# Performance work log

Measured on AMD Instinct MI355X. Metric: run time of the kernel, lower is better.

## Reference

```python
import jax, jax.numpy as jnp
import numpy as np
from jax import lax

MAX_C = 16       # MAX_MERGE_NUMS
COND_THRES = 0.2
IOU_THRES = 0.3
CLASS_OFFSET = 1e4  # shift per-class so cross-class BEV IoU == 0 (emulates per-class loop)


def setup_inputs() -> dict:
    key = jax.random.key(0)
    k1, k2, k3, k4, k5 = jax.random.split(key, 5)
    B, N = 4, 4096
    # realistic 3D boxes: centers, positive sizes, heading
    centers = jax.random.normal(k1, (B, N, 3), jnp.float32) * 20.0
    sizes = jax.random.uniform(k2, (B, N, 3), jnp.float32, 0.5, 4.5)
    heading = jax.random.uniform(k3, (B, N, 1), jnp.float32, -np.pi, np.pi)
    boxes = jnp.concatenate([centers, sizes, heading], -1)  # [B,N,7]
    scores = jax.random.uniform(k4, (B, N), jnp.float32)
    labels = jax.random.randint(k5, (B, N), 0, 3, jnp.int32)
    kw = jax.random.split(jax.random.fold_in(key, 1), 2)
    W1 = jax.random.normal(kw[0], (7, 64), jnp.float32) * 0.3
    b1 = jnp.zeros((64,), jnp.float32)
    W2 = jax.random.normal(kw[1], (64, 1), jnp.float32) * 0.3
    b2 = jnp.zeros((1,), jnp.float32)
    return {"boxes": boxes, "scores": scores, "labels": labels,
            "W1": W1, "b1": b1, "W2": W2, "b2": b2}


def _nms_merge_frame(boxes, scores, labels, W1, b1, W2, b2):
    # boxes [N,7], scores [N], labels [N] int32
    N = boxes.shape[0]
    valid = scores > COND_THRES                       # cond_mask
    skey = jnp.where(valid, scores, -jnp.inf)
    order = jnp.argsort(-skey)                        # score descending
    boxes, scores = boxes[order], scores[order]
    labels, valid = labels[order], valid[order]

    # nearest-BEV (axis-aligned) IoU; class offset keeps classes disjoint
    off = labels.astype(boxes.dtype) * CLASS_OFFSET
    cx, cy = boxes[:, 0] + off, boxes[:, 1]
    hx, hy = boxes[:, 3] * 0.5, boxes[:, 4] * 0.5
    x1, x2, y1, y2 = cx - hx, cx + hx, cy - hy, cy + hy
    ix = jnp.clip(jnp.minimum(x2[:, None], x2[None]) - jnp.maximum(x1[:, None], x1[None]), 0.0)
    iy = jnp.clip(jnp.minimum(y2[:, None], y2[None]) - jnp.maximum(y1[:, None], y1[None]), 0.0)
    inter = ix * iy                                   # [N,N]
    area = (x2 - x1) * (y2 - y1)
    iou = inter / jnp.clip(area[:, None] + area[None] - inter, 1e-6)
    overlap = iou > IOU_THRES                         # includes self

    # greedy clustering: highest-score remaining box leads its cluster
    def body(i, st):
        alive, cid = st
        lead = alive[i]
        take = alive & overlap[i] & lead
        cid = jnp.where(take, i, cid)
        return alive & (~take), cid
    alive, cid = lax.fori_loop(0, N, body,
                               (valid, jnp.full((N,), -1, jnp.int32)))
    leader = cid == jnp.arange(N, dtype=jnp.int32)    # cluster representatives

    # rank of each box within its cluster (score order preserved)
    idx = jnp.arange(N)
    same = (cid[None, :] == cid[:, None]) & (cid[:, None] >= 0)
    rank = (same & (idx[None, :] < idx[:, None])).sum(-1)  # [N]

    # scatter up to MAX_C members per cluster (zero-padded buffers)
    dest = jnp.where((cid >= 0) & (rank < MAX_C), cid, N)  # N = dump row
    clusters = jnp.zeros((N + 1, MAX_C, 7), boxes.dtype)
    clusters = clusters.at[dest, jnp.minimum(rank, MAX_C - 1)].set(boxes)[:N]

    # merge network: per-box MLP -> softmax weights over cluster slots
    h = jax.nn.relu(clusters @ W1 + b1)               # [N,MAX_C,64]
    logits = (h @ W2 + b2)[..., 0]                    # [N,MAX_C]
    slot_ok = jnp.any(clusters != 0, -1)
    logits = jnp.where(slot_ok, logits, -1e9)
    w = jax.nn.softmax(logits, -1)
    merged = jnp.einsum('nc,ncd->nd', w, clusters)    # [N,7]

    # masked scatter: non-positive merged sizes fall back to leader sizes
    size = jnp.where(merged[:, 3:6] <= 0, boxes[:, 3:6], merged[:, 3:6])
    out_box = jnp.concatenate([merged[:, :3], size, merged[:, 6:7]], -1)
    info = jnp.concatenate([out_box, scores[:, None],
                            labels.astype(boxes.dtype)[:, None]], -1)  # [N,9]
    info = jnp.where(leader[:, None], info, 0.0)
    return info, leader


def reference(boxes, scores, labels, W1, b1, W2, b2):
    info, leader = jax.vmap(_nms_merge_frame,
                            in_axes=(0, 0, 0, None, None, None, None))(
        boxes, scores, labels, W1, b1, W2, b2)
    return info, leader
```

## Files before the change

### kernel.cpp

```cpp
#include <hip/hip_runtime.h>
#include <stdint.h>

#pragma clang fp contract(off)

#define BF 4
#define NN 4096
#define MAXC 16
#define PL 2048
#define WL 32
#define WF 24
#define TRI_CAP (64 * (WL * (WL + 1) / 2))

typedef unsigned long long u64;
typedef uint32_t u32;

#define WAVE_SYNC() asm volatile("s_waitcnt lgkmcnt(0)" ::: "memory")

__device__ __forceinline__ u64 shfl64(u64 v, int src) {
  return (u64)__shfl((long long)v, src, 64);
}
__device__ __forceinline__ u64 readlane64(u64 v, int l) {
  u32 lo = (u32)__builtin_amdgcn_readlane((int)(u32)v, l);
  u32 hi = (u32)__builtin_amdgcn_readlane((int)(u32)(v >> 32), l);
  return ((u64)hi << 32) | lo;
}
__device__ __forceinline__ u64 greedy64_iso(u64 D, u64 rem, u64 onlyme) {
  u64 lead = 0;
  while (rem) {
    u64 t = D & rem;
    u64 iso = __ballot(t == onlyme) & rem;
    lead |= iso;
    rem &= ~iso;
    if (!rem) break;
    int b = __builtin_ctzll(rem);
    lead |= 1ull << b;
    rem &= ~readlane64(D, b);
    if (!rem) break;
    b = __builtin_ctzll(rem);
    lead |= 1ull << b;
    rem &= ~readlane64(D, b);
  }
  return lead;
}

__global__ __launch_bounds__(256) void rg_kernel(
    const float* __restrict__ scores, const float* __restrict__ boxes,
    const int* __restrict__ labels,
    float* __restrict__ sboxes, float* __restrict__ sscore, float* __restrict__ slabel,
    int* __restrict__ lab_slot, int* __restrict__ loc_slot,
    int* __restrict__ pglob,
    float* __restrict__ px1, float* __restrict__ px2, float* __restrict__ py1,
    float* __restrict__ py2, float* __restrict__ parea,
    int* __restrict__ VbufL)
{
  __shared__ u64 keys[NN];
  __shared__ int cnt[4][64];
  __shared__ int lcnt[4][64];
  __shared__ int vc[4][3];
  const int f = blockIdx.x >> 6, rb = blockIdx.x & 63;
  const int tid = threadIdx.x, wave = tid >> 6, lane = tid & 63;
  for (int s = 0; s < 16; s++) {
    int idx = tid + 256 * s;
    float sc = scores[f * NN + idx];
    bool valid = sc > 0.2f;
    int lab = labels[f * NN + idx];
    u32 bits = __float_as_uint(sc);
    u32 m = bits ^ ((bits >> 31) ? 0xFFFFFFFFu : 0x80000000u);
    u32 hi = valid ? ~m : 0xFFFFFFFFu;
    u32 lo = ((u32)idx << 2) | (valid ? (u32)lab : 3u);
    keys[idx] = ((u64)hi << 32) | lo;
  }
  __syncthreads();
  if (rb == 0) {
    int c0 = 0, c1 = 0, c2 = 0;
    const int base = wave * 1024;
    for (int s = 0; s < 16; s++) {
      u32 lb = (u32)keys[base + s * 64 + lane] & 3u;
      c0 += (lb == 0); c1 += (lb == 1); c2 += (lb == 2);
    }
    for (int off = 32; off; off >>= 1) {
      c0 += __shfl_xor(c0, off, 64);
      c1 += __shfl_xor(c1, off, 64);
      c2 += __shfl_xor(c2, off, 64);
    }
    if (lane == 0) { vc[wave][0] = c0; vc[wave][1] = c1; vc[wave][2] = c2; }
  }
  const int row = rb * 64 + lane;
  const u64 mykey = keys[row];
  const u32 mylab = (u32)mykey & 3u;
  int c = 0, lc = 0;
  const int j0 = wave * 1024;
#pragma unroll 8
  for (int j = j0; j < j0 + 1024; j++) {
    u64 kj = keys[j];
    bool lt = kj < mykey;
    c += lt ? 1 : 0;
    lc += (lt && (((u32)kj & 3u) == mylab)) ? 1 : 0;
  }
  cnt[wave][lane] = c;
  lcnt[wave][lane] = lc;
  __syncthreads();
  if (rb == 0 && wave == 1 && lane < 3)
    VbufL[f * 3 + lane] = vc[0][lane] + vc[1][lane] + vc[2][lane] + vc[3][lane];
  if (wave == 0) {
    int rank = cnt[0][lane] + cnt[1][lane] + cnt[2][lane] + cnt[3][lane];
    int loc  = lcnt[0][lane] + lcnt[1][lane] + lcnt[2][lane] + lcnt[3][lane];
    const int i = row;
    const float* bp = boxes + (size_t)(f * NN + i) * 7;
    float b0 = bp[0], b1v = bp[1], b2v = bp[2], b3 = bp[3], b4 = bp[4], b5 = bp[5], b6 = bp[6];
    int lab = labels[f * NN + i];
    float sc = scores[f * NN + i];
    const int o = f * NN + rank;
    float* sb = sboxes + (size_t)o * 7;
    sb[0] = b0; sb[1] = b1v; sb[2] = b2v; sb[3] = b3; sb[4] = b4; sb[5] = b5; sb[6] = b6;
    sscore[o] = sc;
    slabel[o] = (float)lab;
    if (mylab < 3u) {
      int pi = (f * 3 + (int)mylab) * PL + loc;
      float off = (float)mylab * 10000.0f;
      float cx = b0 + off, cy = b1v;
      float hx = b3 * 0.5f, hy = b4 * 0.5f;
      float x1 = cx - hx, x2 = cx + hx, y1 = cy - hy, y2 = cy + hy;
      float area = (x2 - x1) * (y2 - y1);
      pglob[pi] = rank;
      px1[pi] = x1; px2[pi] = x2; py1[pi] = y1; py2[pi] = y2; parea[pi] = area;
      lab_slot[o] = (int)mylab; loc_slot[o] = loc;
    } else {
      lab_slot[o] = -1; loc_slot[o] = -1;
    }
  }
}

__global__ __launch_bounds__(256) void mask_kernel(
    const float* __restrict__ px1, const float* __restrict__ px2,
    const float* __restrict__ py1, const float* __restrict__ py2,
    const float* __restrict__ parea, const int* __restrict__ pglob,
    const int* __restrict__ VbufL,
    u64* __restrict__ maskP, u64* __restrict__ triT)
{
  __shared__ float4 cbox[1024];
  __shared__ float carea[1024];
  const int bx = blockIdx.x;
  const int fl = bx >> 8, rem = bx & 255;
  const int rt = rem >> 1, wt = rem & 1;
  const int r0 = rt * 16;
  const int Vl = VbufL[fl];
  if (r0 >= Vl) return;
  if (wt * 1024 >= Vl) return;
  const int tid = threadIdx.x;
  const int ncol = Vl - wt * 1024;
  const int nload = (ncol < 1024) ? ncol : 1024;
  for (int q = tid; q < nload; q += 256) {
    int c = fl * PL + wt * 1024 + q;
    cbox[q] = make_float4(px1[c], px2[c], py1[c], py2[c]);
    carea[q] = parea[c];
  }
  __syncthreads();
  const int row = r0 + (tid & 15);
  const int wl = tid >> 4;
  const int cw = wt * 16 + wl;
  const int nc = Vl - cw * 64;
  if (row >= Vl || nc <= 0) return;
  const int rg = fl * PL + row;
  const float rx1 = px1[rg], rx2 = px2[rg], ry1 = py1[rg], ry2 = py2[rg], ra = parea[rg];
  u64 bits = 0;
  const int qb = wl * 64;
  for (int b = 0; b < 64; b++) {
    float4 cb = cbox[qb + b];
    float ca = carea[qb + b];
    float ix = fminf(rx2, cb.y) - fmaxf(rx1, cb.x);
    ix = fmaxf(ix, 0.0f);
    float iy = fminf(ry2, cb.w) - fmaxf(ry1, cb.z);
    iy = fmaxf(iy, 0.0f);
    float inter = ix * iy;
    float den = fmaxf((ra + ca) - inter, 1e-6f);
    float iou = inter / den;
    bits |= ((u64)(iou > 0.3f)) << b;
  }
  if (nc < 64) bits &= (1ull << nc) - 1ull;
  const int f = fl / 3;
  const int p = pglob[fl * PL + row];
  maskP[((size_t)f * NN + p) * WL + cw] = bits;
  if (row >= 64 * cw) {
    const int W = (Vl + 63) >> 6;
    int base = 64 * (cw * W - (cw * (cw - 1)) / 2);
    triT[(size_t)fl * TRI_CAP + base + (row - 64 * cw)] = bits;
  }
}

__global__ __launch_bounds__(64) void nms_kernel(
    const u64* __restrict__ triT, const int* __restrict__ VbufL,
    u64* __restrict__ leadersP)
{
  __shared__ u64 tri[64 * (WF * (WF + 1) / 2) + 128];
  const int fl = blockIdx.x, lane = threadIdx.x;
  const int Vl = VbufL[fl];
  const int W = (Vl + 63) >> 6;
  const u64* mT = triT + (size_t)fl * TRI_CAP;
  const u64 onlyme = 1ull << lane;
  u64 alive = 0;
  if (lane < WL) {
    int rb = Vl - 64 * lane;
    alive = (rb >= 64) ? ~0ull : ((rb > 0) ? ((1ull << rb) - 1ull) : 0ull);
  }
  u64 myLead = 0;

  if (W > 0 && W <= WF) {
    const int totw = 64 * (W * (W + 1) / 2);
    const int nch = (totw * 8 + 1023) >> 10;
    const char* g = (const char*)mT;
    char* l = (char*)tri;
    int batch = 0;
    for (int it = 0; it < nch; it++) {
      __builtin_amdgcn_global_load_lds(
          (const __attribute__((address_space(1))) unsigned int*)(g + (size_t)it * 1024 + (size_t)lane * 16),
          (__attribute__((address_space(3))) unsigned int*)(l + (size_t)it * 1024),
          16, 0, 0);
      if (++batch == 48) {
        asm volatile("s_waitcnt vmcnt(0)" ::: "memory");
        batch = 0;
      }
    }
    asm volatile("s_waitcnt vmcnt(0)" ::: "memory");
    int offw = 0;
    u64 D = tri[lane];
    for (int w = 0; w < W; w++) {
      const int offw_next = offw + 64 * (W - w);
      u64 Dnext = (w + 1 < W) ? tri[offw_next + lane] : 0;
      u64 lead = greedy64_iso(D, readlane64(alive, w), onlyme);
      if (lane == w) myLead = lead;
      if (lead) {
        const u64* strm = tri + offw;
        int v = w + 1;
        for (; v + 3 < W; v += 4) {
          u64 a0 = strm[64 * (v - w) + lane];
          u64 a1 = strm[64 * (v + 1 - w) + lane];
          u64 a2 = strm[64 * (v + 2 - w) + lane];
          u64 a3 = strm[64 * (v + 3 - w) + lane];
          u64 c0 = __ballot((a0 & lead) != 0ull);
          u64 c1 = __ballot((a1 & lead) != 0ull);
          u64 c2 = __ballot((a2 & lead) != 0ull);
          u64 c3 = __ballot((a3 & lead) != 0ull);
          if (lane == v)     alive &= ~c0;
          if (lane == v + 1) alive &= ~c1;
          if (lane == v + 2) alive &= ~c2;
          if (lane == v + 3) alive &= ~c3;
        }
        for (; v < W; v++) {
          u64 a0 = strm[64 * (v - w) + lane];
          u64 c0 = __ballot((a0 & lead) != 0ull);
          if (lane == v) alive &= ~c0;
        }
      }
      D = Dnext;
      offw = offw_next;
    }
  } else if (W > 0) {
    int offw = 0;
    for (int w = 0; w < W; w++) {
      const u64* strm = mT + offw;
      u64 D = strm[lane];
      u64 lead = greedy64_iso(D, readlane64(alive, w), onlyme);
      if (lane == w) myLead = lead;
      if (lead) {
        for (int v = w + 1; v < W; v++) {
          u64 a0 = strm[64 * (v - w) + lane];
          u64 c0 = __ballot((a0 & lead) != 0ull);
          if (lane == v) alive &= ~c0;
        }
      }
      offw += 64 * (W - w);
    }
  }
  if (lane < WL) leadersP[fl * WL + lane] = myLead;
}

__global__ __launch_bounds__(256) void cid_kernel(
    const u64* __restrict__ maskP, const u64* __restrict__ leadersP,
    const int* __restrict__ lab_slot, const int* __restrict__ loc_slot,
    const int* __restrict__ VbufL, int* __restrict__ cidP)
{
  const int g = blockIdx.x * 4 + (threadIdx.x >> 6);
  const int lane = threadIdx.x & 63;
  const int f = g >> 12, p = g & (NN - 1);
  const int l = lab_slot[f * NN + p];
  if (l < 0) return;
  const int fl = f * 3 + l;
  const int loc = loc_slot[f * NN + p];
  const int Wl = (VbufL[fl] + 63) >> 6;
  u64 L = 0, m = 0;
  if (lane < Wl) {
    L = leadersP[fl * WL + lane];
    m = maskP[((size_t)f * NN + p) * WL + lane];
  }
  const int g6 = loc >> 6, b6 = loc & 63;
  u64 pmask = (lane < g6) ? ~0ull
            : (lane == g6 ? ((b6 == 63) ? ~0ull : ((1ull << (b6 + 1)) - 1ull)) : 0ull);
  u64 v = m & L & pmask;
  u64 bl = __ballot(v != 0ull);
  int cid = -1;
  if (bl != 0ull) {
    int w = __builtin_ctzll(bl);
    u64 vw = shfl64(v, w);
    cid = w * 64 + __builtin_ctzll(vw);
  }
  if (lane == 0) cidP[fl * PL + loc] = cid;
}

__global__ __launch_bounds__(256) void mm_kernel(
    const u64* __restrict__ maskP, const u64* __restrict__ leadersP,
    const int* __restrict__ cidP, const int* __restrict__ lab_slot,
    const int* __restrict__ loc_slot, const int* __restrict__ pglob,
    const int* __restrict__ VbufL,
    const float* __restrict__ sboxes, const float* __restrict__ sscore,
    const float* __restrict__ slabel,
    const float* __restrict__ W1, const float* __restrict__ b1,
    const float* __restrict__ W2, const float* __restrict__ b2,
    float* __restrict__ out)
{
  __shared__ int   mlistS[4][MAXC];
  __shared__ float mbS[4][MAXC][7];
  __shared__ float lgS[4][MAXC];
  __shared__ float wnS[4][MAXC];
  const int wv = threadIdx.x >> 6, lane = threadIdx.x & 63;
  const int bi = blockIdx.x * 4 + wv;
  const int f = bi >> 12, i = bi & (NN - 1);
  const int o = f * NN + i;
  float* info = out + (size_t)o * 9;
  float* lead = out + (size_t)BF * NN * 9 + o;
  const int l = lab_slot[o];
  bool isLead = false;
  int loc = 0, fl = 0;
  if (l >= 0) {
    fl = f * 3 + l;
    loc = loc_slot[o];
    isLead = (leadersP[fl * WL + (loc >> 6)] >> (loc & 63)) & 1ull;
  }
  if (!isLead) {
    if (lane < 9) info[lane] = 0.0f;
    if (lane == 0) *lead = 0.0f;
    return;
  }
  int* mlist = mlistS[wv];
  float (*mb)[7] = mbS[wv];
  float* lg = lgS[wv];
  float* wn = wnS[wv];
  const u64* mrow = maskP + (size_t)o * WL;
  const int Wl = (VbufL[fl] + 63) >> 6;
  int total = 0;
  for (int w = loc >> 6; w < Wl && total < MAXC; w++) {
    u64 word = mrow[w];
    int pos = w * 64 + lane;
    bool cand = ((word >> lane) & 1ull) && (cidP[fl * PL + pos] == loc);
    u64 mbal = __ballot(cand);
    int r = __popcll(mbal & ((1ull << lane) - 1ull));
    int slot = total + r;
    if (cand && slot < MAXC) mlist[slot] = pglob[fl * PL + pos];
    total += __popcll(mbal);
  }
  const int cnt = min(total, MAXC);
  WAVE_SYNC();
  if (lane < cnt) {
    int j = mlist[lane];
    const float* bp = sboxes + (size_t)(f * NN + j) * 7;
    for (int d = 0; d < 7; d++) mb[lane][d] = bp[d];
  }
  float w1r[7];
  for (int d = 0; d < 7; d++) w1r[d] = W1[d * 64 + lane];
  const float b1c = b1[lane], w2c = W2[lane], b2v = b2[0];
  WAVE_SYNC();
  for (int s = 0; s < cnt; s++) {
    float t = b1c;
    for (int d = 0; d < 7; d++) t += mb[s][d] * w1r[d];
    float h = fmaxf(t, 0.0f);
    float v = h * w2c;
    for (int off2 = 32; off2 > 0; off2 >>= 1) v += __shfl_xor(v, off2, 64);
    if (lane == 0) lg[s] = v + b2v;
  }
  WAVE_SYNC();
  float mx = -1e30f;
  for (int s = 0; s < cnt; s++) mx = fmaxf(mx, lg[s]);
  float den = 0.0f;
  for (int s = 0; s < cnt; s++) den += expf(lg[s] - mx);
  if (lane < cnt) wn[lane] = expf(lg[lane] - mx) / den;
  WAVE_SYNC();
  float val = 0.0f;
  if (lane < 7) {
    float acc = 0.0f;
    for (int s = 0; s < cnt; s++) acc += wn[s] * mb[s][lane];
    val = acc;
    if (lane >= 3 && lane <= 5 && val <= 0.0f) val = sboxes[(size_t)o * 7 + lane];
  } else if (lane == 7) {
    val = sscore[o];
  } else if (lane == 8) {
    val = slabel[o];
  }
  if (lane < 9) info[lane] = val;
  if (lane == 0) *lead = 1.0f;
}

extern "C" void kernel_launch(void* const* d_in, const int* in_sizes, int n_in,
                              void* d_out, int out_size, void* d_ws, size_t ws_size,
                              hipStream_t stream)
{
  const float* boxes  = (const float*)d_in[0];
  const float* scores = (const float*)d_in[1];
  const int*   labels = (const int*)d_in[2];
  const float* W1     = (const float*)d_in[3];
  const float* b1     = (const float*)d_in[4];
  const float* W2     = (const float*)d_in[5];
  const float* b2     = (const float*)d_in[6];
  float* out = (float*)d_out;

  char* ws = (char*)d_ws;
  size_t off = 0;
  auto alloc = [&](size_t bytes) -> void* {
    void* p = ws + off;
    off = (off + bytes + 255) & ~(size_t)255;
    return p;
  };
  float* sboxes  = (float*)alloc((size_t)BF * NN * 7 * 4);
  float* sscore  = (float*)alloc((size_t)BF * NN * 4);
  float* slabel  = (float*)alloc((size_t)BF * NN * 4);
  int*   lab_slot= (int*)  alloc((size_t)BF * NN * 4);
  int*   loc_slot= (int*)  alloc((size_t)BF * NN * 4);
  int*   pglob   = (int*)  alloc((size_t)BF * 3 * PL * 4);
  float* px1     = (float*)alloc((size_t)BF * 3 * PL * 4);
  float* px2     = (float*)alloc((size_t)BF * 3 * PL * 4);
  float* py1     = (float*)alloc((size_t)BF * 3 * PL * 4);
  float* py2     = (float*)alloc((size_t)BF * 3 * PL * 4);
  float* parea   = (float*)alloc((size_t)BF * 3 * PL * 4);
  int*   VbufL   = (int*)  alloc((size_t)BF * 3 * 4);
  u64*   leadersP= (u64*)  alloc((size_t)BF * 3 * WL * 8);
  int*   cidP    = (int*)  alloc((size_t)BF * 3 * PL * 4);
  u64*   maskP   = (u64*)  alloc((size_t)BF * NN * WL * 8);
  u64*   triT    = (u64*)  alloc((size_t)BF * 3 * TRI_CAP * 8);
  (void)  alloc(32768);

  rg_kernel<<<BF * 64, 256, 0, stream>>>(scores, boxes, labels, sboxes,
                                         sscore, slabel, lab_slot, loc_slot,
                                         pglob, px1, px2, py1, py2, parea,
                                         VbufL);
  mask_kernel<<<BF * 3 * 256, 256, 0, stream>>>(px1, px2, py1, py2, parea,
                                                pglob, VbufL, maskP, triT);
  nms_kernel<<<BF * 3, 64, 0, stream>>>(triT, VbufL, leadersP);
  cid_kernel<<<BF * NN / 4, 256, 0, stream>>>(maskP, leadersP, lab_slot,
                                              loc_slot, VbufL, cidP);
  mm_kernel<<<BF * NN / 4, 256, 0, stream>>>(maskP, leadersP, cidP, lab_slot,
                                             loc_slot, pglob, VbufL, sboxes,
                                             sscore, slabel, W1, b1, W2, b2, out);
}
```

Before: 156.8 us.

## Compact leader list in NMS kernel and run merge only over leaders

```diff
diff --git a/kernel.cpp b/kernel.cpp
--- a/kernel.cpp
+++ b/kernel.cpp
@@ -88,6 +88,8 @@
   const int row = rb * 64 + lane;
   const u64 mykey = keys[row];
   const u32 mylab = (u32)mykey & 3u;
+  const u64 ltmask = (1ull << lane) - 1ull;
+  (void)ltmask;
   int c = 0, lc = 0;
   const int j0 = wave * 1024;
 #pragma unroll 8
@@ -190,7 +192,8 @@
 
 __global__ __launch_bounds__(64) void nms_kernel(
     const u64* __restrict__ triT, const int* __restrict__ VbufL,
-    u64* __restrict__ leadersP)
+    const int* __restrict__ pglob,
+    u64* __restrict__ leadersP, int2* __restrict__ llist, int* __restrict__ lcount)
 {
   __shared__ u64 tri[64 * (WF * (WF + 1) / 2) + 128];
   const int fl = blockIdx.x, lane = threadIdx.x;
@@ -273,6 +276,28 @@
     }
   }
   if (lane < WL) leadersP[fl * WL + lane] = myLead;
+
+  int nl = __popcll(myLead);
+  int incl = nl;
+  for (int off = 1; off < 64; off <<= 1) {
+    int up = __shfl_up(incl, off, 64);
+    if (lane >= off) incl += up;
+  }
+  int tot = __shfl(incl, 63, 64);
+  int base = 0;
+  if (lane == 0 && tot > 0) base = atomicAdd(lcount, tot);
+  base = __shfl(base, 0, 64);
+  int start = base + incl - nl;
+  const int f = fl / 3;
+  u64 m = myLead;
+  while (m) {
+    int b = __builtin_ctzll(m);
+    m &= m - 1;
+    int pos = 64 * lane + b;
+    int p = pglob[fl * PL + pos];
+    llist[start] = make_int2(f * NN + p, (fl << 16) | pos);
+    start++;
+  }
 }
 
 __global__ __launch_bounds__(256) void cid_kernel(
@@ -308,10 +333,9 @@
 }
 
 __global__ __launch_bounds__(256) void mm_kernel(
-    const u64* __restrict__ maskP, const u64* __restrict__ leadersP,
-    const int* __restrict__ cidP, const int* __restrict__ lab_slot,
-    const int* __restrict__ loc_slot, const int* __restrict__ pglob,
-    const int* __restrict__ VbufL,
+    const int2* __restrict__ llist, const int* __restrict__ lcount,
+    const u64* __restrict__ maskP, const int* __restrict__ cidP,
+    const int* __restrict__ pglob, const int* __restrict__ VbufL,
     const float* __restrict__ sboxes, const float* __restrict__ sscore,
     const float* __restrict__ slabel,
     const float* __restrict__ W1, const float* __restrict__ b1,
@@ -323,80 +347,73 @@
   __shared__ float lgS[4][MAXC];
   __shared__ float wnS[4][MAXC];
   const int wv = threadIdx.x >> 6, lane = threadIdx.x & 63;
-  const int bi = blockIdx.x * 4 + wv;
-  const int f = bi >> 12, i = bi & (NN - 1);
-  const int o = f * NN + i;
-  float* info = out + (size_t)o * 9;
-  float* lead = out + (size_t)BF * NN * 9 + o;
-  const int l = lab_slot[o];
-  bool isLead = false;
-  int loc = 0, fl = 0;
-  if (l >= 0) {
-    fl = f * 3 + l;
-    loc = loc_slot[o];
-    isLead = (leadersP[fl * WL + (loc >> 6)] >> (loc & 63)) & 1ull;
-  }
-  if (!isLead) {
-    if (lane < 9) info[lane] = 0.0f;
-    if (lane == 0) *lead = 0.0f;
-    return;
-  }
+  const u64 ltmask = (1ull << lane) - 1ull;
   int* mlist = mlistS[wv];
   float (*mb)[7] = mbS[wv];
   float* lg = lgS[wv];
   float* wn = wnS[wv];
-  const u64* mrow = maskP + (size_t)o * WL;
-  const int Wl = (VbufL[fl] + 63) >> 6;
-  int total = 0;
-  for (int w = loc >> 6; w < Wl && total < MAXC; w++) {
-    u64 word = mrow[w];
-    int pos = w * 64 + lane;
-    bool cand = ((word >> lane) & 1ull) && (cidP[fl * PL + pos] == loc);
-    u64 mbal = __ballot(cand);
-    int r = __popcll(mbal & ((1ull << lane) - 1ull));
-    int slot = total + r;
-    if (cand && slot < MAXC) mlist[slot] = pglob[fl * PL + pos];
-    total += __popcll(mbal);
-  }
-  const int cnt = min(total, MAXC);
-  WAVE_SYNC();
-  if (lane < cnt) {
-    int j = mlist[lane];
-    const float* bp = sboxes + (size_t)(f * NN + j) * 7;
-    for (int d = 0; d < 7; d++) mb[lane][d] = bp[d];
-  }
   float w1r[7];
   for (int d = 0; d < 7; d++) w1r[d] = W1[d * 64 + lane];
   const float b1c = b1[lane], w2c = W2[lane], b2v = b2[0];
-  WAVE_SYNC();
-  for (int s = 0; s < cnt; s++) {
-    float t = b1c;
-    for (int d = 0; d < 7; d++) t += mb[s][d] * w1r[d];
-    float h = fmaxf(t, 0.0f);
-    float v = h * w2c;
-    for (int off2 = 32; off2 > 0; off2 >>= 1) v += __shfl_xor(v, off2, 64);
-    if (lane == 0) lg[s] = v + b2v;
-  }
-  WAVE_SYNC();
-  float mx = -1e30f;
-  for (int s = 0; s < cnt; s++) mx = fmaxf(mx, lg[s]);
-  float den = 0.0f;
-  for (int s = 0; s < cnt; s++) den += expf(lg[s] - mx);
-  if (lane < cnt) wn[lane] = expf(lg[lane] - mx) / den;
-  WAVE_SYNC();
-  float val = 0.0f;
-  if (lane < 7) {
-    float acc = 0.0f;
-    for (int s = 0; s < cnt; s++) acc += wn[s] * mb[s][lane];
-    val = acc;
-    if (lane >= 3 && lane <= 5 && val <= 0.0f) val = sboxes[(size_t)o * 7 + lane];
-  } else if (lane == 7) {
-    val = sscore[o];
-  } else if (lane == 8) {
-    val = slabel[o];
-  }
-  if (lane < 9) info[lane] = val;
-  if (lane == 0) *lead = 1.0f;
+  const int cntTot = lcount[0];
+  for (int idx = blockIdx.x * 4 + wv; idx < cntTot; idx += 1024) {
+    int2 e = llist[idx];
+    const int o = e.x;
+    const int fl = e.y >> 16, loc = e.y & 0xFFFF;
+    const int f = o >> 12;
+    float* info = out + (size_t)o * 9;
+    float* lead = out + (size_t)BF * NN * 9 + o;
+    const u64* mrow = maskP + (size_t)o * WL;
+    const int Wl = (VbufL[fl] + 63) >> 6;
+    int total = 0;
+    for (int w = loc >> 6; w < Wl && total < MAXC; w++) {
+      u64 word = mrow[w];
+      int pos = w * 64 + lane;
+      bool cand = ((word >> lane) & 1ull) && (cidP[fl * PL + pos] == loc);
+      u64 mbal = __ballot(cand);
+      int r = __popcll(mbal & ltmask);
+      int slot = total + r;
+      if (cand && slot < MAXC) mlist[slot] = pglob[fl * PL + pos];
+      total += __popcll(mbal);
+    }
+    const int cnt = min(total, MAXC);
+    WAVE_SYNC();
+    if (lane < cnt) {
+      int j = mlist[lane];
+      const float* bp = sboxes + (size_t)(f * NN + j) * 7;
+      for (int d = 0; d < 7; d++) mb[lane][d] = bp[d];
+    }
+    WAVE_SYNC();
+    for (int s = 0; s < cnt; s++) {
+      float t = b1c;
+      for (int d = 0; d < 7; d++) t += mb[s][d] * w1r[d];
+      float h = fmaxf(t, 0.0f);
+      float v = h * w2c;
+      for (int off2 = 32; off2 > 0; off2 >>= 1) v += __shfl_xor(v, off2, 64);
+      if (lane == 0) lg[s] = v + b2v;
+    }
+    WAVE_SYNC();
+    float mx = -1e30f;
+    for (int s = 0; s < cnt; s++) mx = fmaxf(mx, lg[s]);
+    float den = 0.0f;
+    for (int s = 0; s < cnt; s++) den += expf(lg[s] - mx);
+    if (lane < cnt) wn[lane] = expf(lg[lane] - mx) / den;
+    WAVE_SYNC();
+    float val = 0.0f;
+    if (lane < 7) {
+      float acc = 0.0f;
+      for (int s = 0; s < cnt; s++) acc += wn[s] * mb[s][lane];
+      val = acc;
+      if (lane >= 3 && lane <= 5 && val <= 0.0f) val = sboxes[(size_t)o * 7 + lane];
+    } else if (lane == 7) {
+      val = sscore[o];
+    } else if (lane == 8) {
+      val = slabel[o];
+    }
+    if (lane < 9) info[lane] = val;
+    if (lane == 0) *lead = 1.0f;
+    WAVE_SYNC();
+  }
 }
 
 extern "C" void kernel_launch(void* const* d_in, const int* in_sizes, int n_in,
@@ -419,6 +436,8 @@
     off = (off + bytes + 255) & ~(size_t)255;
     return p;
   };
+  int*   lcount  = (int*)  alloc(256);
+  int2*  llist   = (int2*) alloc((size_t)BF * NN * 8);
   float* sboxes  = (float*)alloc((size_t)BF * NN * 7 * 4);
   float* sscore  = (float*)alloc((size_t)BF * NN * 4);
   float* slabel  = (float*)alloc((size_t)BF * NN * 4);
@@ -437,16 +456,20 @@
   u64*   triT    = (u64*)  alloc((size_t)BF * 3 * TRI_CAP * 8);
   (void)  alloc(32768);
 
+  hipMemsetAsync(lcount, 0, 256, stream);
+  hipMemsetAsync(d_out, 0, (size_t)out_size * 4, stream);
+
   rg_kernel<<<BF * 64, 256, 0, stream>>>(scores, boxes, labels, sboxes,
                                          sscore, slabel, lab_slot, loc_slot,
                                          pglob, px1, px2, py1, py2, parea,
                                          VbufL);
   mask_kernel<<<BF * 3 * 256, 256, 0, stream>>>(px1, px2, py1, py2, parea,
                                                 pglob, VbufL, maskP, triT);
-  nms_kernel<<<BF * 3, 64, 0, stream>>>(triT, VbufL, leadersP);
+  nms_kernel<<<BF * 3, 64, 0, stream>>>(triT, VbufL, pglob, leadersP,
+                                        llist, lcount);
   cid_kernel<<<BF * NN / 4, 256, 0, stream>>>(maskP, leadersP, lab_slot,
                                               loc_slot, VbufL, cidP);
-  mm_kernel<<<BF * NN / 4, 256, 0, stream>>>(maskP, leadersP, cidP, lab_slot,
-                                             loc_slot, pglob, VbufL, sboxes,
-                                             sscore, slabel, W1, b1, W2, b2, out);
-}
+  mm_kernel<<<256, 256, 0, stream>>>(llist, lcount, maskP, cidP, pglob,
+                                     VbufL, sboxes, sscore, slabel,
+                                     W1, b1, W2, b2, out);
+}
```

Result: slower. 212.2 us (+35.3%).
